# Kernel tuning notes

Measured on AMD Instinct MI355X. Metric: run time of the kernel, lower is better.

Reference implementation:

```python
import jax, jax.numpy as jnp
import numpy as np

N_NODES = 50000
N_EDGES = 800000
IN_FEATS = 128
HIDDEN = 256
N_CLASSES = 64


def setup_inputs() -> dict:
    key = jax.random.key(0)
    ks = jax.random.split(key, 16)
    def w(k, shape, fan_in):
        return jax.random.normal(k, shape, dtype=jnp.float32) * (1.0 / np.sqrt(fan_in))
    inp = {
        "x": jax.random.normal(ks[0], (N_NODES, IN_FEATS), dtype=jnp.float32),
        "edge_src": jax.random.randint(ks[1], (N_EDGES,), 0, N_NODES, dtype=jnp.int32),
        "edge_dst": jax.random.randint(ks[2], (N_EDGES,), 0, N_NODES, dtype=jnp.int32),
        # layer 0: in_feats -> hidden
        "W0s": w(ks[3], (IN_FEATS, HIDDEN), IN_FEATS),
        "W0n": w(ks[4], (IN_FEATS, HIDDEN), IN_FEATS),
        "b0": jnp.zeros((HIDDEN,), dtype=jnp.float32),
        # layer 1: hidden -> hidden
        "W1s": w(ks[5], (HIDDEN, HIDDEN), HIDDEN),
        "W1n": w(ks[6], (HIDDEN, HIDDEN), HIDDEN),
        "b1": jnp.zeros((HIDDEN,), dtype=jnp.float32),
        # layer 2: hidden -> hidden (last conv also outputs hidden per source code)
        "W2s": w(ks[7], (HIDDEN, HIDDEN), HIDDEN),
        "W2n": w(ks[8], (HIDDEN, HIDDEN), HIDDEN),
        "b2": jnp.zeros((HIDDEN,), dtype=jnp.float32),
        # fc1: hidden -> n_classes
        "Wfc": w(ks[9], (HIDDEN, N_CLASSES), HIDDEN),
        "bfc": jnp.zeros((N_CLASSES,), dtype=jnp.float32),
    }
    return inp


def _sage_layer(h, src, dst, Ws, Wn, b):
    # mean-neighbor aggregation: segment-sum messages, divide by in-degree
    msg = h[src]  # [E, D] irregular gather
    agg = jax.ops.segment_sum(msg, dst, num_segments=N_NODES)  # [N, D]
    deg = jax.ops.segment_sum(jnp.ones_like(dst, dtype=h.dtype), dst, num_segments=N_NODES)
    h_neigh = agg / jnp.maximum(deg, 1.0)[:, None]
    # DGL SAGEConv (mean): fc_self(h) + fc_neigh(h_neigh) + bias
    return h @ Ws + h_neigh @ Wn + b


def reference(x, edge_src, edge_dst, W0s, W0n, b0, W1s, W1n, b1, W2s, W2n, b2, Wfc, bfc):
    # forward applies dropout (identity at eval) and NO activation between layers,
    # matching the original module's forward().
    h = _sage_layer(x, edge_src, edge_dst, W0s, W0n, b0)
    h = _sage_layer(h, edge_src, edge_dst, W1s, W1n, b1)
    h = _sage_layer(h, edge_src, edge_dst, W2s, W2n, b2)
    return h @ Wfc + bfc  # [N, n_classes]
```

## Files before the change

kernel.cpp:

```cpp
#include <hip/hip_runtime.h>

#define NN 50000
#define NE 800000
#define F_IN 128
#define HID 256
#define N_CLS 64
#define SCAN_BLOCKS ((NN + 255) / 256)
#define CROWS 515

typedef _Float16 half8 __attribute__((ext_vector_type(8)));
typedef float f32x4 __attribute__((ext_vector_type(4)));

__global__ void hist_count(const int* __restrict__ dst, int* __restrict__ cnt,
                           int* __restrict__ rank, int E) {
    int i = blockIdx.x * blockDim.x + threadIdx.x;
    if (i < E) rank[i] = atomicAdd(&cnt[dst[i]], 1);
}

__global__ void scan_block_sums(const int* __restrict__ cnt, int* __restrict__ blockSums, int n) {
    __shared__ int s[256];
    int t = threadIdx.x;
    int i = blockIdx.x * 256 + t;
    s[t] = (i < n) ? cnt[i] : 0;
    __syncthreads();
    for (int off = 128; off > 0; off >>= 1) {
        if (t < off) s[t] += s[t + off];
        __syncthreads();
    }
    if (t == 0) blockSums[blockIdx.x] = s[0];
}

__global__ void scan_top(int* __restrict__ blockSums, int nb) {
    __shared__ int s[256];
    int t = threadIdx.x;
    s[t] = (t < nb) ? blockSums[t] : 0;
    __syncthreads();
    for (int off = 1; off < 256; off <<= 1) {
        int v = (t >= off) ? s[t - off] : 0;
        __syncthreads();
        s[t] += v;
        __syncthreads();
    }
    if (t < nb) blockSums[t] = (t > 0) ? s[t - 1] : 0;
}

__global__ void scan_final(const int* __restrict__ cnt, const int* __restrict__ blockBase,
                           int* __restrict__ offs, float* __restrict__ dinv, int n) {
    __shared__ int s[256];
    int t = threadIdx.x;
    int i = blockIdx.x * 256 + t;
    int v = (i < n) ? cnt[i] : 0;
    s[t] = v;
    __syncthreads();
    for (int off = 1; off < 256; off <<= 1) {
        int u = (t >= off) ? s[t - off] : 0;
        __syncthreads();
        s[t] += u;
        __syncthreads();
    }
    if (i < n) {
        offs[i] = blockBase[blockIdx.x] + s[t] - v;
        dinv[i] = 1.0f / (float)max(v, 1);
    }
    if (i == n - 1) offs[n] = blockBase[blockIdx.x] + s[t];
}

__global__ void csr_place2(const int* __restrict__ src, const int* __restrict__ dst,
                           const int* __restrict__ rank, const int* __restrict__ offs,
                           unsigned short* __restrict__ csr, int E) {
    int e = blockIdx.x * blockDim.x + threadIdx.x;
    if (e < E) csr[offs[dst[e]] + rank[e]] = (unsigned short)src[e];
}

__device__ __forceinline__ const float* virtC1_row(int r, const float* W0s,
                                                   const float* W0n, const float* b0) {
    if (r < 0) return nullptr;
    if (r < 128) return W0s + (size_t)r * 256;
    if (r < 256) return W0n + (size_t)(r - 128) * 256;
    if (r == 512) return b0;
    return nullptr;
}

__device__ __forceinline__ int shift_src(int r) {
    if (r >= 128 && r < 512) return r - 128;
    if (r == 513) return 512;
    if (r == 514) return 513;
    return -1;
}

__global__ __launch_bounds__(256) void gemm_compose_first(
    const float* __restrict__ W0s, const float* __restrict__ W0n, const float* __restrict__ b0,
    const float* __restrict__ B1, const float* __restrict__ B2,
    const float* __restrict__ brow, float* __restrict__ C)
{
    __shared__ float As[64][17];
    __shared__ float Bs[16][64];
    const int tid = threadIdx.x;
    const int tx = tid & 15, ty = tid >> 4;
    const int row0 = blockIdx.x * 64;
    const int col0 = blockIdx.y * 64;
    const int lr = tid >> 2, lc = tid & 3;
    const int br = tid >> 4, bc = tid & 15;

    float acc[4][4] = {};

    for (int pass = 0; pass < 2; ++pass) {
        const float* B = pass ? B2 : B1;
        int grow = row0 + lr;
        int srcr = pass ? shift_src(grow) : (grow < CROWS ? grow : -1);
        const float* ap = virtC1_row(srcr, W0s, W0n, b0);

        for (int k0 = 0; k0 < 256; k0 += 16) {
            float4 av = make_float4(0.f, 0.f, 0.f, 0.f);
            if (ap) av = *(const float4*)(ap + k0 + lc * 4);
            As[lr][lc * 4 + 0] = av.x;
            As[lr][lc * 4 + 1] = av.y;
            As[lr][lc * 4 + 2] = av.z;
            As[lr][lc * 4 + 3] = av.w;
            *(float4*)&Bs[br][bc * 4] = *(const float4*)(B + (size_t)(k0 + br) * 256 + col0 + bc * 4);
            __syncthreads();
            #pragma unroll
            for (int k = 0; k < 16; ++k) {
                float a[4];
                #pragma unroll
                for (int i = 0; i < 4; ++i) a[i] = As[ty * 4 + i][k];
                float4 bv = *(const float4*)&Bs[k][tx * 4];
                const float b[4] = {bv.x, bv.y, bv.z, bv.w};
                #pragma unroll
                for (int i = 0; i < 4; ++i)
                    #pragma unroll
                    for (int j = 0; j < 4; ++j)
                        acc[i][j] += a[i] * b[j];
            }
            __syncthreads();
        }
    }

    #pragma unroll
    for (int i = 0; i < 4; ++i) {
        int r = row0 + ty * 4 + i;
        if (r < CROWS) {
            #pragma unroll
            for (int j = 0; j < 4; ++j) {
                float v = acc[i][j];
                if (r == 512) v += brow[col0 + tx * 4 + j];
                C[(size_t)r * 256 + col0 + tx * 4 + j] = v;
            }
        }
    }
}

__global__ __launch_bounds__(256) void gemm_compose_mid(
    const float* __restrict__ A,
    const float* __restrict__ B1, const float* __restrict__ B2,
    const float* __restrict__ brow, float* __restrict__ C)
{
    __shared__ float As[64][17];
    __shared__ float Bs[16][64];
    const int tid = threadIdx.x;
    const int tx = tid & 15, ty = tid >> 4;
    const int row0 = blockIdx.x * 64;
    const int col0 = blockIdx.y * 64;
    const int lr = tid >> 2, lc = tid & 3;
    const int br = tid >> 4, bc = tid & 15;

    float acc[4][4] = {};

    for (int pass = 0; pass < 2; ++pass) {
        const float* B = pass ? B2 : B1;
        int grow = row0 + lr;
        int p = pass ? shift_src(grow) : (grow < CROWS ? grow : -1);

        for (int k0 = 0; k0 < 256; k0 += 16) {
            float4 av = make_float4(0.f, 0.f, 0.f, 0.f);
            if (p >= 0) av = *(const float4*)(A + (size_t)p * 256 + k0 + lc * 4);
            As[lr][lc * 4 + 0] = av.x;
            As[lr][lc * 4 + 1] = av.y;
            As[lr][lc * 4 + 2] = av.z;
            As[lr][lc * 4 + 3] = av.w;
            *(float4*)&Bs[br][bc * 4] = *(const float4*)(B + (size_t)(k0 + br) * 256 + col0 + bc * 4);
            __syncthreads();
            #pragma unroll
            for (int k = 0; k < 16; ++k) {
                float a[4];
                #pragma unroll
                for (int i = 0; i < 4; ++i) a[i] = As[ty * 4 + i][k];
                float4 bv = *(const float4*)&Bs[k][tx * 4];
                const float b[4] = {bv.x, bv.y, bv.z, bv.w};
                #pragma unroll
                for (int i = 0; i < 4; ++i)
                    #pragma unroll
                    for (int j = 0; j < 4; ++j)
                        acc[i][j] += a[i] * b[j];
            }
            __syncthreads();
        }
    }

    #pragma unroll
    for (int i = 0; i < 4; ++i) {
        int r = row0 + ty * 4 + i;
        if (r < CROWS) {
            #pragma unroll
            for (int j = 0; j < 4; ++j) {
                float v = acc[i][j];
                if (r == 512) v += brow[col0 + tx * 4 + j];
                C[(size_t)r * 256 + col0 + tx * 4 + j] = v;
            }
        }
    }
}

__global__ __launch_bounds__(256) void gemm_compose_last(
    const float* __restrict__ A, const float* __restrict__ B1,
    const float* __restrict__ brow, float* __restrict__ Vf, _Float16* __restrict__ BT)
{
    __shared__ float As[64][17];
    __shared__ float Bs[16][64];
    const int tid = threadIdx.x;
    const int tx = tid & 15, ty = tid >> 4;
    const int row0 = blockIdx.x * 64;
    const int lr = tid >> 2, lc = tid & 3;
    const int br = tid >> 4, bc = tid & 15;

    float acc[4][4] = {};

    for (int k0 = 0; k0 < 256; k0 += 16) {
        float4 av = make_float4(0.f, 0.f, 0.f, 0.f);
        int grow = row0 + lr;
        if (grow < CROWS) av = *(const float4*)(A + (size_t)grow * 256 + k0 + lc * 4);
        As[lr][lc * 4 + 0] = av.x;
        As[lr][lc * 4 + 1] = av.y;
        As[lr][lc * 4 + 2] = av.z;
        As[lr][lc * 4 + 3] = av.w;
        *(float4*)&Bs[br][bc * 4] = *(const float4*)(B1 + (size_t)(k0 + br) * 64 + bc * 4);
        __syncthreads();
        #pragma unroll
        for (int k = 0; k < 16; ++k) {
            float a[4];
            #pragma unroll
            for (int i = 0; i < 4; ++i) a[i] = As[ty * 4 + i][k];
            float4 bv = *(const float4*)&Bs[k][tx * 4];
            const float b[4] = {bv.x, bv.y, bv.z, bv.w};
            #pragma unroll
            for (int i = 0; i < 4; ++i)
                #pragma unroll
                for (int j = 0; j < 4; ++j)
                    acc[i][j] += a[i] * b[j];
        }
        __syncthreads();
    }

    #pragma unroll
    for (int i = 0; i < 4; ++i) {
        int r = row0 + ty * 4 + i;
        if (r < CROWS) {
            #pragma unroll
            for (int j = 0; j < 4; ++j) {
                int c = tx * 4 + j;
                float v = acc[i][j];
                if (r == 512) v += brow[c];
                Vf[(size_t)r * 64 + c] = v;
                if (r < 512)
                    BT[(size_t)((r >> 7) * 64 + c) * 128 + (r & 127)] = (_Float16)v;
            }
        }
    }
}

__global__ __launch_bounds__(256) void gemm_Y(
    const float* __restrict__ X, const _Float16* __restrict__ BT,
    _Float16* __restrict__ Y, int N)
{
    constexpr int LP = 40;
    __shared__ _Float16 As[128 * LP];
    __shared__ _Float16 Bs[128 * LP];

    const int tid = threadIdx.x;
    const int wave = tid >> 6;
    const int lane = tid & 63;
    const int l15 = lane & 15;
    const int quad = lane >> 4;
    const int wrow = wave >> 1;
    const int wcol = wave & 1;
    const int m_base = wrow * 64;
    const int n_base = wcol * 64;

    const int row0 = blockIdx.x * 128;
    const int col0 = blockIdx.y * 128;

    f32x4 acc[4][4] = {};

    for (int k0 = 0; k0 < 128; k0 += 32) {
        #pragma unroll
        for (int r = 0; r < 2; ++r) {
            int idx = r * 256 + tid;
            int row = idx >> 2, ch = idx & 3;
            int gr = row0 + row; if (gr > N - 1) gr = N - 1;
            const float* ap = X + (size_t)gr * 128 + k0 + ch * 8;
            float4 f0 = *(const float4*)ap;
            float4 f1 = *(const float4*)(ap + 4);
            half8 v = { (_Float16)f0.x, (_Float16)f0.y, (_Float16)f0.z, (_Float16)f0.w,
                        (_Float16)f1.x, (_Float16)f1.y, (_Float16)f1.z, (_Float16)f1.w };
            *(half8*)&As[row * LP + ch * 8] = v;
        }
        #pragma unroll
        for (int r = 0; r < 2; ++r) {
            int idx = r * 256 + tid;
            int row = idx >> 2, ch = idx & 3;
            *(half8*)&Bs[row * LP + ch * 8] =
                *(const half8*)(BT + (size_t)(col0 + row) * 128 + k0 + ch * 8);
        }
        __syncthreads();
        half8 af[4], bf[4];
        #pragma unroll
        for (int i = 0; i < 4; ++i)
            af[i] = *(const half8*)&As[(m_base + i * 16 + l15) * LP + quad * 8];
        #pragma unroll
        for (int j = 0; j < 4; ++j)
            bf[j] = *(const half8*)&Bs[(n_base + j * 16 + l15) * LP + quad * 8];
        #pragma unroll
        for (int i = 0; i < 4; ++i)
            #pragma unroll
            for (int j = 0; j < 4; ++j)
                acc[i][j] = __builtin_amdgcn_mfma_f32_16x16x32_f16(af[i], bf[j], acc[i][j], 0, 0, 0);
        __syncthreads();
    }

    #pragma unroll
    for (int i = 0; i < 4; ++i) {
        #pragma unroll
        for (int j = 0; j < 4; ++j) {
            int col = col0 + n_base + j * 16 + l15;
            #pragma unroll
            for (int r = 0; r < 4; ++r) {
                int row = row0 + m_base + i * 16 + quad * 4 + r;
                if (row < N)
                    Y[(size_t)row * 256 + col] = (_Float16)acc[i][j][r];
            }
        }
    }
}

template <bool OUT_F32>
__global__ __launch_bounds__(256) void gather64(
    const _Float16* __restrict__ Tin, int sin,
    const unsigned short* __restrict__ csr, const int* __restrict__ offs,
    const float* __restrict__ dinv,
    const _Float16* __restrict__ Yadd,
    const float* __restrict__ cvec,
    void* __restrict__ Tout, int N)
{
    int node = blockIdx.x * 32 + (threadIdx.x >> 3);
    int lane = threadIdx.x & 7;
    if (node >= N) return;
    int beg = offs[node], end = offs[node + 1];
    float acc[8] = {};
    int e = beg;
    for (; e + 3 < end; e += 4) {
        int s0 = csr[e], s1 = csr[e + 1], s2 = csr[e + 2], s3 = csr[e + 3];
        half8 v0 = *(const half8*)(Tin + (size_t)s0 * sin + lane * 8);
        half8 v1 = *(const half8*)(Tin + (size_t)s1 * sin + lane * 8);
        half8 v2 = *(const half8*)(Tin + (size_t)s2 * sin + lane * 8);
        half8 v3 = *(const half8*)(Tin + (size_t)s3 * sin + lane * 8);
        #pragma unroll
        for (int j = 0; j < 8; ++j)
            acc[j] += ((float)v0[j] + (float)v1[j]) + ((float)v2[j] + (float)v3[j]);
    }
    for (; e < end; ++e) {
        half8 v = *(const half8*)(Tin + (size_t)csr[e] * sin + lane * 8);
        #pragma unroll
        for (int j = 0; j < 8; ++j) acc[j] += (float)v[j];
    }
    float sc = dinv[node];
    half8 y = *(const half8*)(Yadd + (size_t)node * 256 + lane * 8);
    if (OUT_F32) {
        float* o = (float*)Tout + (size_t)node * 64 + lane * 8;
        float4 o0, o1;
        o0.x = acc[0] * sc + (float)y[0] + cvec[lane * 8 + 0];
        o0.y = acc[1] * sc + (float)y[1] + cvec[lane * 8 + 1];
        o0.z = acc[2] * sc + (float)y[2] + cvec[lane * 8 + 2];
        o0.w = acc[3] * sc + (float)y[3] + cvec[lane * 8 + 3];
        o1.x = acc[4] * sc + (float)y[4] + cvec[lane * 8 + 4];
        o1.y = acc[5] * sc + (float)y[5] + cvec[lane * 8 + 5];
        o1.z = acc[6] * sc + (float)y[6] + cvec[lane * 8 + 6];
        o1.w = acc[7] * sc + (float)y[7] + cvec[lane * 8 + 7];
        *(float4*)o = o0;
        *(float4*)(o + 4) = o1;
    } else {
        half8 o;
        #pragma unroll
        for (int j = 0; j < 8; ++j)
            o[j] = (_Float16)(acc[j] * sc + (float)y[j] + cvec[lane * 8 + j]);
        *(half8*)((_Float16*)Tout + (size_t)node * 64 + lane * 8) = o;
    }
}

extern "C" void kernel_launch(void* const* d_in, const int* in_sizes, int n_in,
                              void* d_out, int out_size, void* d_ws, size_t ws_size,
                              hipStream_t stream) {
    const float* x    = (const float*)d_in[0];
    const int*   esrc = (const int*)d_in[1];
    const int*   edst = (const int*)d_in[2];
    const float* W0s  = (const float*)d_in[3];
    const float* W0n  = (const float*)d_in[4];
    const float* b0   = (const float*)d_in[5];
    const float* W1s  = (const float*)d_in[6];
    const float* W1n  = (const float*)d_in[7];
    const float* b1   = (const float*)d_in[8];
    const float* W2s  = (const float*)d_in[9];
    const float* W2n  = (const float*)d_in[10];
    const float* b2   = (const float*)d_in[11];
    const float* Wfc  = (const float*)d_in[12];
    const float* bfc  = (const float*)d_in[13];
    float* out = (float*)d_out;

    _Float16* Y   = (_Float16*)d_ws;
    _Float16* Ta  = Y + (size_t)NN * 256;
    _Float16* Tb  = Ta + (size_t)NN * 64;
    _Float16* BT  = Tb + (size_t)NN * 64;
    float* C2     = (float*)(BT + 256 * 128);
    float* C3     = C2 + CROWS * 256;
    float* Vf     = C3 + CROWS * 256;
    float* dinv   = Vf + CROWS * 64;
    int* cnt      = (int*)(dinv + NN);
    int* offs     = cnt + NN;
    int* rank     = offs + NN + 1;
    int* blockSums = rank + NE;
    unsigned short* csr = (unsigned short*)(blockSums + SCAN_BLOCKS);

    hipMemsetAsync(cnt, 0, (size_t)NN * sizeof(int), stream);
    hist_count<<<(NE + 255) / 256, 256, 0, stream>>>(edst, cnt, rank, NE);
    scan_block_sums<<<SCAN_BLOCKS, 256, 0, stream>>>(cnt, blockSums, NN);
    scan_top<<<1, 256, 0, stream>>>(blockSums, SCAN_BLOCKS);
    scan_final<<<SCAN_BLOCKS, 256, 0, stream>>>(cnt, blockSums, offs, dinv, NN);
    csr_place2<<<(NE + 255) / 256, 256, 0, stream>>>(esrc, edst, rank, offs, csr, NE);

    const int gR = (CROWS + 63) / 64;
    gemm_compose_first<<<dim3(gR, 4), 256, 0, stream>>>(W0s, W0n, b0, W1s, W1n, b1, C2);
    gemm_compose_mid<<<dim3(gR, 4), 256, 0, stream>>>(C2, W2s, W2n, b2, C3);
    gemm_compose_last<<<dim3(gR, 1), 256, 0, stream>>>(C3, Wfc, bfc, Vf, BT);

    gemm_Y<<<dim3((NN + 127) / 128, 2), 256, 0, stream>>>(x, BT, Y, NN);

    const int ggrid = (NN + 31) / 32;
    gather64<false><<<ggrid, 256, 0, stream>>>(
        Y + 192, 256, csr, offs, dinv, Y + 128, Vf + (size_t)514 * 64, Ta, NN);
    gather64<false><<<ggrid, 256, 0, stream>>>(
        Ta, 64, csr, offs, dinv, Y + 64, Vf + (size_t)513 * 64, Tb, NN);
    gather64<true><<<ggrid, 256, 0, stream>>>(
        Tb, 64, csr, offs, dinv, Y, Vf + (size_t)512 * 64, out, NN);
}
```

Baseline: 301.5 us.

## Sort nodes by in-degree for load-balanced gathers and shrink rank to ushort

Builds a degree histogram during the scan, prefix-sums the bins in descending order, and writes a node permutation grouped by in-degree. The three gather kernels then process nodes in that order, so wavefronts see similar edge counts and spend less time idle on divergent loops. The rank array is also narrowed to 16-bit to cut memory traffic in CSR construction. It adds two small kernels and an extra indirection, and output writes become scattered rather than contiguous.

```diff
diff --git a/kernel.cpp b/kernel.cpp
--- a/kernel.cpp
+++ b/kernel.cpp
@@ -12,9 +12,9 @@
 typedef float f32x4 __attribute__((ext_vector_type(4)));
 
 __global__ void hist_count(const int* __restrict__ dst, int* __restrict__ cnt,
-                           int* __restrict__ rank, int E) {
+                           unsigned short* __restrict__ rank, int E) {
     int i = blockIdx.x * blockDim.x + threadIdx.x;
-    if (i < E) rank[i] = atomicAdd(&cnt[dst[i]], 1);
+    if (i < E) rank[i] = (unsigned short)atomicAdd(&cnt[dst[i]], 1);
 }
 
 __global__ void scan_block_sums(const int* __restrict__ cnt, int* __restrict__ blockSums, int n) {
@@ -45,9 +45,12 @@
 }
 
 __global__ void scan_final(const int* __restrict__ cnt, const int* __restrict__ blockBase,
-                           int* __restrict__ offs, float* __restrict__ dinv, int n) {
+                           int* __restrict__ offs, float* __restrict__ dinv,
+                           int* __restrict__ dbin, int n) {
     __shared__ int s[256];
+    __shared__ int hb[256];
     int t = threadIdx.x;
+    hb[t] = 0;
     int i = blockIdx.x * 256 + t;
     int v = (i < n) ? cnt[i] : 0;
     s[t] = v;
@@ -61,12 +64,50 @@
     if (i < n) {
         offs[i] = blockBase[blockIdx.x] + s[t] - v;
         dinv[i] = 1.0f / (float)max(v, 1);
+        atomicAdd(&hb[min(v, 255)], 1);
     }
     if (i == n - 1) offs[n] = blockBase[blockIdx.x] + s[t];
+    __syncthreads();
+    if (hb[t]) atomicAdd(&dbin[t], hb[t]);
+}
+
+__global__ void bin_scan(const int* __restrict__ dbin, int* __restrict__ dcur) {
+    __shared__ int s[256];
+    int t = threadIdx.x;
+    int v0 = dbin[t];
+    s[t] = v0;
+    __syncthreads();
+    for (int off = 1; off < 256; off <<= 1) {
+        int u = (t >= off) ? s[t - off] : 0;
+        __syncthreads();
+        s[t] += u;
+        __syncthreads();
+    }
+    int total = s[255];
+    dcur[t] = total - s[t];
+}
+
+__global__ void perm_place(const int* __restrict__ cnt, int* __restrict__ dcur,
+                           int* __restrict__ perm, int n) {
+    __shared__ int hb[256];
+    __shared__ int base[256];
+    int t = threadIdx.x;
+    hb[t] = 0;
+    __syncthreads();
+    int i = blockIdx.x * 256 + t;
+    int b = -1, lr = 0;
+    if (i < n) {
+        b = min(cnt[i], 255);
+        lr = atomicAdd(&hb[b], 1);
+    }
+    __syncthreads();
+    if (hb[t]) base[t] = atomicAdd(&dcur[t], hb[t]);
+    __syncthreads();
+    if (i < n) perm[base[b] + lr] = i;
 }
 
 __global__ void csr_place2(const int* __restrict__ src, const int* __restrict__ dst,
-                           const int* __restrict__ rank, const int* __restrict__ offs,
+                           const unsigned short* __restrict__ rank, const int* __restrict__ offs,
                            unsigned short* __restrict__ csr, int E) {
     int e = blockIdx.x * blockDim.x + threadIdx.x;
     if (e < E) csr[offs[dst[e]] + rank[e]] = (unsigned short)src[e];
@@ -346,14 +387,16 @@
 __global__ __launch_bounds__(256) void gather64(
     const _Float16* __restrict__ Tin, int sin,
     const unsigned short* __restrict__ csr, const int* __restrict__ offs,
+    const int* __restrict__ perm,
     const float* __restrict__ dinv,
     const _Float16* __restrict__ Yadd,
     const float* __restrict__ cvec,
     void* __restrict__ Tout, int N)
 {
-    int node = blockIdx.x * 32 + (threadIdx.x >> 3);
+    int slot = blockIdx.x * 32 + (threadIdx.x >> 3);
     int lane = threadIdx.x & 7;
-    if (node >= N) return;
+    if (slot >= N) return;
+    int node = perm[slot];
     int beg = offs[node], end = offs[node + 1];
     float acc[8] = {};
     int e = beg;
@@ -424,16 +467,21 @@
     float* Vf     = C3 + CROWS * 256;
     float* dinv   = Vf + CROWS * 64;
     int* cnt      = (int*)(dinv + NN);
-    int* offs     = cnt + NN;
-    int* rank     = offs + NN + 1;
-    int* blockSums = rank + NE;
-    unsigned short* csr = (unsigned short*)(blockSums + SCAN_BLOCKS);
-
-    hipMemsetAsync(cnt, 0, (size_t)NN * sizeof(int), stream);
+    int* dbin     = cnt + NN;
+    int* dcur     = dbin + 256;
+    int* offs     = dcur + 256;
+    int* perm     = offs + NN + 1;
+    int* blockSums = perm + NN;
+    unsigned short* rank = (unsigned short*)(blockSums + SCAN_BLOCKS);
+    unsigned short* csr  = rank + NE;
+
+    hipMemsetAsync(cnt, 0, (size_t)(NN + 512) * sizeof(int), stream);
     hist_count<<<(NE + 255) / 256, 256, 0, stream>>>(edst, cnt, rank, NE);
     scan_block_sums<<<SCAN_BLOCKS, 256, 0, stream>>>(cnt, blockSums, NN);
     scan_top<<<1, 256, 0, stream>>>(blockSums, SCAN_BLOCKS);
-    scan_final<<<SCAN_BLOCKS, 256, 0, stream>>>(cnt, blockSums, offs, dinv, NN);
+    scan_final<<<SCAN_BLOCKS, 256, 0, stream>>>(cnt, blockSums, offs, dinv, dbin, NN);
+    bin_scan<<<1, 256, 0, stream>>>(dbin, dcur);
+    perm_place<<<SCAN_BLOCKS, 256, 0, stream>>>(cnt, dcur, perm, NN);
     csr_place2<<<(NE + 255) / 256, 256, 0, stream>>>(esrc, edst, rank, offs, csr, NE);
 
     const int gR = (CROWS + 63) / 64;
@@ -445,9 +493,9 @@
 
     const int ggrid = (NN + 31) / 32;
     gather64<false><<<ggrid, 256, 0, stream>>>(
-        Y + 192, 256, csr, offs, dinv, Y + 128, Vf + (size_t)514 * 64, Ta, NN);
+        Y + 192, 256, csr, offs, perm, dinv, Y + 128, Vf + (size_t)514 * 64, Ta, NN);
     gather64<false><<<ggrid, 256, 0, stream>>>(
-        Ta, 64, csr, offs, dinv, Y + 64, Vf + (size_t)513 * 64, Tb, NN);
+        Ta, 64, csr, offs, perm, dinv, Y + 64, Vf + (size_t)513 * 64, Tb, NN);
     gather64<true><<<ggrid, 256, 0, stream>>>(
-        Tb, 64, csr, offs, dinv, Y, Vf + (size_t)512 * 64, out, NN);
-}
+        Tb, 64, csr, offs, perm, dinv, Y, Vf + (size_t)512 * 64, out, NN);
+}
```

New measurement: 309.0 us. 2.5% more time.

## Fuse scan stages with weight-compose GEMMs and compact gather source layout

Applied to the files above, without the earlier changes.

Merges the three prefix-scan kernels with the three weight-composition GEMM kernels into three combined launches that split work by block index, cutting the number of launches. The rank array shrinks from int to 16-bit, reducing memory traffic in the histogram and CSR placement. gemm_Y also writes a contiguous 64-wide copy of its last column slice, so the first gather reads dense rows instead of strided 256-wide rows. The trade-off is an extra write in gemm_Y, and a 16-bit rank that assumes no node has more than 65535 incoming edges.

```diff
diff --git a/kernel.cpp b/kernel.cpp
--- a/kernel.cpp
+++ b/kernel.cpp
@@ -12,12 +12,13 @@
 typedef float f32x4 __attribute__((ext_vector_type(4)));
 
 __global__ void hist_count(const int* __restrict__ dst, int* __restrict__ cnt,
-                           int* __restrict__ rank, int E) {
+                           unsigned short* __restrict__ rank, int E) {
     int i = blockIdx.x * blockDim.x + threadIdx.x;
-    if (i < E) rank[i] = atomicAdd(&cnt[dst[i]], 1);
-}
-
-__global__ void scan_block_sums(const int* __restrict__ cnt, int* __restrict__ blockSums, int n) {
+    if (i < E) rank[i] = (unsigned short)atomicAdd(&cnt[dst[i]], 1);
+}
+
+__device__ __forceinline__ void scan_block_sums_dev(const int* __restrict__ cnt,
+                                                    int* __restrict__ blockSums, int n) {
     __shared__ int s[256];
     int t = threadIdx.x;
     int i = blockIdx.x * 256 + t;
@@ -30,7 +31,7 @@
     if (t == 0) blockSums[blockIdx.x] = s[0];
 }
 
-__global__ void scan_top(int* __restrict__ blockSums, int nb) {
+__device__ __forceinline__ void scan_top_dev(int* __restrict__ blockSums, int nb) {
     __shared__ int s[256];
     int t = threadIdx.x;
     s[t] = (t < nb) ? blockSums[t] : 0;
@@ -44,8 +45,10 @@
     if (t < nb) blockSums[t] = (t > 0) ? s[t - 1] : 0;
 }
 
-__global__ void scan_final(const int* __restrict__ cnt, const int* __restrict__ blockBase,
-                           int* __restrict__ offs, float* __restrict__ dinv, int n) {
+__device__ __forceinline__ void scan_final_dev(const int* __restrict__ cnt,
+                                               const int* __restrict__ blockBase,
+                                               int* __restrict__ offs,
+                                               float* __restrict__ dinv, int n) {
     __shared__ int s[256];
     int t = threadIdx.x;
     int i = blockIdx.x * 256 + t;
@@ -66,7 +69,7 @@
 }
 
 __global__ void csr_place2(const int* __restrict__ src, const int* __restrict__ dst,
-                           const int* __restrict__ rank, const int* __restrict__ offs,
+                           const unsigned short* __restrict__ rank, const int* __restrict__ offs,
                            unsigned short* __restrict__ csr, int E) {
     int e = blockIdx.x * blockDim.x + threadIdx.x;
     if (e < E) csr[offs[dst[e]] + rank[e]] = (unsigned short)src[e];
@@ -88,8 +91,10 @@
     return -1;
 }
 
-__global__ __launch_bounds__(256) void gemm_compose_first(
-    const float* __restrict__ W0s, const float* __restrict__ W0n, const float* __restrict__ b0,
+
+__device__ __forceinline__ void compose_first_dev(
+    int bx, const float* __restrict__ W0s, const float* __restrict__ W0n,
+    const float* __restrict__ b0,
     const float* __restrict__ B1, const float* __restrict__ B2,
     const float* __restrict__ brow, float* __restrict__ C)
 {
@@ -97,8 +102,8 @@
     __shared__ float Bs[16][64];
     const int tid = threadIdx.x;
     const int tx = tid & 15, ty = tid >> 4;
-    const int row0 = blockIdx.x * 64;
-    const int col0 = blockIdx.y * 64;
+    const int row0 = (bx % 9) * 64;
+    const int col0 = (bx / 9) * 64;
     const int lr = tid >> 2, lc = tid & 3;
     const int br = tid >> 4, bc = tid & 15;
 
@@ -150,8 +155,8 @@
     }
 }
 
-__global__ __launch_bounds__(256) void gemm_compose_mid(
-    const float* __restrict__ A,
+__device__ __forceinline__ void compose_mid_dev(
+    int bx, const float* __restrict__ A,
     const float* __restrict__ B1, const float* __restrict__ B2,
     const float* __restrict__ brow, float* __restrict__ C)
 {
@@ -159,8 +164,8 @@
     __shared__ float Bs[16][64];
     const int tid = threadIdx.x;
     const int tx = tid & 15, ty = tid >> 4;
-    const int row0 = blockIdx.x * 64;
-    const int col0 = blockIdx.y * 64;
+    const int row0 = (bx % 9) * 64;
+    const int col0 = (bx / 9) * 64;
     const int lr = tid >> 2, lc = tid & 3;
     const int br = tid >> 4, bc = tid & 15;
 
@@ -211,15 +216,15 @@
     }
 }
 
-__global__ __launch_bounds__(256) void gemm_compose_last(
-    const float* __restrict__ A, const float* __restrict__ B1,
+__device__ __forceinline__ void compose_last_dev(
+    int bx, const float* __restrict__ A, const float* __restrict__ B1,
     const float* __restrict__ brow, float* __restrict__ Vf, _Float16* __restrict__ BT)
 {
     __shared__ float As[64][17];
     __shared__ float Bs[16][64];
     const int tid = threadIdx.x;
     const int tx = tid & 15, ty = tid >> 4;
-    const int row0 = blockIdx.x * 64;
+    const int row0 = bx * 64;
     const int lr = tid >> 2, lc = tid & 3;
     const int br = tid >> 4, bc = tid & 15;
 
@@ -268,9 +273,39 @@
     }
 }
 
+__global__ __launch_bounds__(256) void k_scanA_composeF(
+    const int* __restrict__ cnt, int* __restrict__ blockSums,
+    const float* __restrict__ W0s, const float* __restrict__ W0n, const float* __restrict__ b0,
+    const float* __restrict__ W1s, const float* __restrict__ W1n, const float* __restrict__ b1,
+    float* __restrict__ C2)
+{
+    if (blockIdx.x < SCAN_BLOCKS) scan_block_sums_dev(cnt, blockSums, NN);
+    else compose_first_dev(blockIdx.x - SCAN_BLOCKS, W0s, W0n, b0, W1s, W1n, b1, C2);
+}
+
+__global__ __launch_bounds__(256) void k_scanT_composeM(
+    int* __restrict__ blockSums,
+    const float* __restrict__ C2,
+    const float* __restrict__ W2s, const float* __restrict__ W2n, const float* __restrict__ b2,
+    float* __restrict__ C3)
+{
+    if (blockIdx.x == 0) scan_top_dev(blockSums, SCAN_BLOCKS);
+    else compose_mid_dev(blockIdx.x - 1, C2, W2s, W2n, b2, C3);
+}
+
+__global__ __launch_bounds__(256) void k_scanF_composeL(
+    const int* __restrict__ cnt, const int* __restrict__ blockBase,
+    int* __restrict__ offs, float* __restrict__ dinv,
+    const float* __restrict__ C3, const float* __restrict__ Wfc, const float* __restrict__ bfc,
+    float* __restrict__ Vf, _Float16* __restrict__ BT)
+{
+    if (blockIdx.x < SCAN_BLOCKS) scan_final_dev(cnt, blockBase, offs, dinv, NN);
+    else compose_last_dev(blockIdx.x - SCAN_BLOCKS, C3, Wfc, bfc, Vf, BT);
+}
+
 __global__ __launch_bounds__(256) void gemm_Y(
     const float* __restrict__ X, const _Float16* __restrict__ BT,
-    _Float16* __restrict__ Y, int N)
+    _Float16* __restrict__ Y, _Float16* __restrict__ Tc, int N)
 {
     constexpr int LP = 40;
     __shared__ _Float16 As[128 * LP];
@@ -335,8 +370,11 @@
             #pragma unroll
             for (int r = 0; r < 4; ++r) {
                 int row = row0 + m_base + i * 16 + quad * 4 + r;
-                if (row < N)
-                    Y[(size_t)row * 256 + col] = (_Float16)acc[i][j][r];
+                if (row < N) {
+                    _Float16 v = (_Float16)acc[i][j][r];
+                    Y[(size_t)row * 256 + col] = v;
+                    if (col >= 192) Tc[(size_t)row * 64 + (col - 192)] = v;
+                }
             }
         }
     }
@@ -344,7 +382,7 @@
 
 template <bool OUT_F32>
 __global__ __launch_bounds__(256) void gather64(
-    const _Float16* __restrict__ Tin, int sin,
+    const _Float16* __restrict__ Tin,
     const unsigned short* __restrict__ csr, const int* __restrict__ offs,
     const float* __restrict__ dinv,
     const _Float16* __restrict__ Yadd,
@@ -359,16 +397,16 @@
     int e = beg;
     for (; e + 3 < end; e += 4) {
         int s0 = csr[e], s1 = csr[e + 1], s2 = csr[e + 2], s3 = csr[e + 3];
-        half8 v0 = *(const half8*)(Tin + (size_t)s0 * sin + lane * 8);
-        half8 v1 = *(const half8*)(Tin + (size_t)s1 * sin + lane * 8);
-        half8 v2 = *(const half8*)(Tin + (size_t)s2 * sin + lane * 8);
-        half8 v3 = *(const half8*)(Tin + (size_t)s3 * sin + lane * 8);
+        half8 v0 = *(const half8*)(Tin + (size_t)s0 * 64 + lane * 8);
+        half8 v1 = *(const half8*)(Tin + (size_t)s1 * 64 + lane * 8);
+        half8 v2 = *(const half8*)(Tin + (size_t)s2 * 64 + lane * 8);
+        half8 v3 = *(const half8*)(Tin + (size_t)s3 * 64 + lane * 8);
         #pragma unroll
         for (int j = 0; j < 8; ++j)
             acc[j] += ((float)v0[j] + (float)v1[j]) + ((float)v2[j] + (float)v3[j]);
     }
     for (; e < end; ++e) {
-        half8 v = *(const half8*)(Tin + (size_t)csr[e] * sin + lane * 8);
+        half8 v = *(const half8*)(Tin + (size_t)csr[e] * 64 + lane * 8);
         #pragma unroll
         for (int j = 0; j < 8; ++j) acc[j] += (float)v[j];
     }
@@ -418,36 +456,34 @@
     _Float16* Y   = (_Float16*)d_ws;
     _Float16* Ta  = Y + (size_t)NN * 256;
     _Float16* Tb  = Ta + (size_t)NN * 64;
-    _Float16* BT  = Tb + (size_t)NN * 64;
+    _Float16* Tc  = Tb + (size_t)NN * 64;
+    _Float16* BT  = Tc + (size_t)NN * 64;
     float* C2     = (float*)(BT + 256 * 128);
     float* C3     = C2 + CROWS * 256;
     float* Vf     = C3 + CROWS * 256;
     float* dinv   = Vf + CROWS * 64;
     int* cnt      = (int*)(dinv + NN);
     int* offs     = cnt + NN;
-    int* rank     = offs + NN + 1;
-    int* blockSums = rank + NE;
-    unsigned short* csr = (unsigned short*)(blockSums + SCAN_BLOCKS);
+    int* blockSums = offs + NN + 1;
+    unsigned short* rank = (unsigned short*)(blockSums + SCAN_BLOCKS);
+    unsigned short* csr  = rank + NE;
 
     hipMemsetAsync(cnt, 0, (size_t)NN * sizeof(int), stream);
     hist_count<<<(NE + 255) / 256, 256, 0, stream>>>(edst, cnt, rank, NE);
-    scan_block_sums<<<SCAN_BLOCKS, 256, 0, stream>>>(cnt, blockSums, NN);
-    scan_top<<<1, 256, 0, stream>>>(blockSums, SCAN_BLOCKS);
-    scan_final<<<SCAN_BLOCKS, 256, 0, stream>>>(cnt, blockSums, offs, dinv, NN);
+    k_scanA_composeF<<<SCAN_BLOCKS + 36, 256, 0, stream>>>(
+        cnt, blockSums, W0s, W0n, b0, W1s, W1n, b1, C2);
+    k_scanT_composeM<<<1 + 36, 256, 0, stream>>>(blockSums, C2, W2s, W2n, b2, C3);
+    k_scanF_composeL<<<SCAN_BLOCKS + 9, 256, 0, stream>>>(
+        cnt, blockSums, offs, dinv, C3, Wfc, bfc, Vf, BT);
     csr_place2<<<(NE + 255) / 256, 256, 0, stream>>>(esrc, edst, rank, offs, csr, NE);
 
-    const int gR = (CROWS + 63) / 64;
-    gemm_compose_first<<<dim3(gR, 4), 256, 0, stream>>>(W0s, W0n, b0, W1s, W1n, b1, C2);
-    gemm_compose_mid<<<dim3(gR, 4), 256, 0, stream>>>(C2, W2s, W2n, b2, C3);
-    gemm_compose_last<<<dim3(gR, 1), 256, 0, stream>>>(C3, Wfc, bfc, Vf, BT);
-
-    gemm_Y<<<dim3((NN + 127) / 128, 2), 256, 0, stream>>>(x, BT, Y, NN);
+    gemm_Y<<<dim3((NN + 127) / 128, 2), 256, 0, stream>>>(x, BT, Y, Tc, NN);
 
     const int ggrid = (NN + 31) / 32;
     gather64<false><<<ggrid, 256, 0, stream>>>(
-        Y + 192, 256, csr, offs, dinv, Y + 128, Vf + (size_t)514 * 64, Ta, NN);
+        Tc, csr, offs, dinv, Y + 128, Vf + (size_t)514 * 64, Ta, NN);
     gather64<false><<<ggrid, 256, 0, stream>>>(
-        Ta, 64, csr, offs, dinv, Y + 64, Vf + (size_t)513 * 64, Tb, NN);
+        Ta, csr, offs, dinv, Y + 64, Vf + (size_t)513 * 64, Tb, NN);
     gather64<true><<<ggrid, 256, 0, stream>>>(
-        Tb, 64, csr, offs, dinv, Y, Vf + (size_t)512 * 64, out, NN);
-}
+        Tb, csr, offs, dinv, Y, Vf + (size_t)512 * 64, out, NN);
+}
```

New measurement: 291.3 us. -3.4%, faster.
